# Kernel tuning notes

Hardware: AMD Instinct MI355X
Metric: run time of the kernel (lower is better)

Reference implementation:

```python
import jax, jax.numpy as jnp
import numpy as np

D_MODEL = 768
N_HEADS = 12
D_HEAD = D_MODEL // N_HEADS

def setup_inputs() -> dict:
    key = jax.random.key(0)
    ks = jax.random.split(key, 5)
    B, T = 2, 4096
    x = jax.random.normal(ks[0], (B, T, D_MODEL), dtype=jnp.float32)
    s_in = 1.0 / np.sqrt(D_MODEL)
    W_qkv = jax.random.normal(ks[1], (D_MODEL, 3 * D_MODEL), dtype=jnp.float32) * s_in
    b_qkv = jnp.zeros((3 * D_MODEL,), dtype=jnp.float32)
    W_proj = jax.random.normal(ks[2], (D_MODEL, D_MODEL), dtype=jnp.float32) * s_in
    b_proj = jnp.zeros((D_MODEL,), dtype=jnp.float32)
    return {"x": x, "W_qkv": W_qkv, "b_qkv": b_qkv, "W_proj": W_proj, "b_proj": b_proj}

def reference(x, W_qkv, b_qkv, W_proj, b_proj):
    B, T, C = x.shape
    qkv = x @ W_qkv + b_qkv                      # [B,T,3C]
    q, k, v = jnp.split(qkv, 3, axis=-1)
    def heads(t):
        return t.reshape(B, T, N_HEADS, D_HEAD).transpose(0, 2, 1, 3)  # [B,H,T,d]
    q, k, v = heads(q), heads(k), heads(v)
    scale = 1.0 / np.sqrt(D_HEAD)
    att = jnp.einsum('bhqd,bhkd->bhqk', q, k) * scale  # [B,H,T,T]
    causal = jnp.tril(jnp.ones((T, T), dtype=bool))
    att = jnp.where(causal[None, None], att, -jnp.inf)
    att = jax.nn.softmax(att, axis=-1)
    y = jnp.einsum('bhqk,bhkd->bhqd', att, v)          # [B,H,T,d]
    y = y.transpose(0, 2, 1, 3).reshape(B, T, C)
    return y @ W_proj + b_proj
```

## Files before the change

kernel.cpp:

```cpp
#include <hip/hip_runtime.h>
#include <hip/hip_bf16.h>

typedef __bf16 bf16_t;
typedef bf16_t bf16x4 __attribute__((ext_vector_type(4)));
typedef bf16_t bf16x8 __attribute__((ext_vector_type(8)));
typedef float  f32x4  __attribute__((ext_vector_type(4)));

#define TSEQ   4096
#define NBATCH 2
#define DMODEL 768
#define NHEADS 12
#define DHEAD  64
#define NTOK   (NBATCH*TSEQ)
#define NQKV   (3*DMODEL)

#define QSCALE 0.18033688011112042f
#define SMAX 24.0f

__device__ __forceinline__ f32x4 mfma16(bf16x8 a, bf16x8 b, f32x4 c) {
  return __builtin_amdgcn_mfma_f32_16x16x32_bf16(a, b, c, 0, 0, 0);
}

__device__ __forceinline__ void glds16(const bf16_t* g, bf16_t* l) {
  __builtin_amdgcn_global_load_lds(
      (const __attribute__((address_space(1))) void*)g,
      (__attribute__((address_space(3))) void*)l, 16, 0, 0);
}

__global__ void k_cvt(const float* __restrict__ in, bf16_t* __restrict__ out, int n) {
  int i = blockIdx.x * blockDim.x + threadIdx.x;
  if (i < n) out[i] = (bf16_t)in[i];
}

__global__ __launch_bounds__(256) void k_transpose_cvt(
    const float* __restrict__ in, bf16_t* __restrict__ out, int R, int C) {
  __shared__ bf16_t tile[64][66];
  const int c0 = blockIdx.x * 64, r0 = blockIdx.y * 64;
  const int tid = threadIdx.x;
  const int r = tid >> 2, cb = (tid & 3) * 16;
  const float* ip = in + (long)(r0 + r) * C + c0 + cb;
#pragma unroll
  for (int k = 0; k < 16; k += 4) {
    float4 v = *(const float4*)(ip + k);
    tile[r][cb + k + 0] = (bf16_t)v.x;
    tile[r][cb + k + 1] = (bf16_t)v.y;
    tile[r][cb + k + 2] = (bf16_t)v.z;
    tile[r][cb + k + 3] = (bf16_t)v.w;
  }
  __syncthreads();
  const int c = tid >> 2, rb = (tid & 3) * 16;
  bf16_t* op = out + (long)(c0 + c) * R + r0 + rb;
  bf16x8 v0, v1;
#pragma unroll
  for (int i = 0; i < 8; ++i) { v0[i] = tile[rb + i][c]; v1[i] = tile[rb + 8 + i][c]; }
  *(bf16x8*)(op) = v0;
  *(bf16x8*)(op + 8) = v1;
}

__device__ __forceinline__ void gemm_core(
    const bf16_t* __restrict__ A, const bf16_t* __restrict__ Bt,
    int m0, int n0, bf16_t* As, bf16_t* Bs, f32x4 acc[2][8]) {
  const int tid  = threadIdx.x;
  const int wave = tid >> 6;
  const int lane = tid & 63;
  const int quad = lane >> 4;
  const int l16  = lane & 15;
  const int srow = lane >> 2;
  const int scol = (lane & 3) * 8;

  const bf16_t* a0 = A + (long)(m0 + wave * 16 + srow) * DMODEL + scol;
  const bf16_t* b0 = Bt + (long)(n0 + wave * 16 + srow) * DMODEL + scol;

  glds16(a0,               As + wave * 16 * 32);
  glds16(a0 + 64 * DMODEL, As + (64 + wave * 16) * 32);
  glds16(b0,               Bs + wave * 16 * 32);
  glds16(b0 + 64 * DMODEL, Bs + (64 + wave * 16) * 32);
  __syncthreads();

  for (int ks = 0; ks < DMODEL / 32; ++ks) {
    const int p = ks & 1;
    if (ks + 1 < DMODEL / 32) {
      const int k1 = (ks + 1) * 32;
      bf16_t* Asx = (p ? As : As + 128 * 32);
      bf16_t* Bsx = (p ? Bs : Bs + 128 * 32);
      glds16(a0 + k1,               Asx + wave * 16 * 32);
      glds16(a0 + 64 * DMODEL + k1, Asx + (64 + wave * 16) * 32);
      glds16(b0 + k1,               Bsx + wave * 16 * 32);
      glds16(b0 + 64 * DMODEL + k1, Bsx + (64 + wave * 16) * 32);
    }
    const bf16_t* Ap = As + p * (128 * 32);
    const bf16_t* Bp = Bs + p * (128 * 32);

    bf16x8 af0 = *(const bf16x8*)(Ap + (wave * 32 + l16) * 32 + quad * 8);
    bf16x8 af1 = *(const bf16x8*)(Ap + (wave * 32 + 16 + l16) * 32 + quad * 8);
#pragma unroll
    for (int nt = 0; nt < 8; ++nt) {
      bf16x8 bfm = *(const bf16x8*)(Bp + (nt * 16 + l16) * 32 + quad * 8);
      acc[0][nt] = mfma16(af0, bfm, acc[0][nt]);
      acc[1][nt] = mfma16(af1, bfm, acc[1][nt]);
    }
    __syncthreads();
  }
}

__global__ __launch_bounds__(256) void k_gemm_qkv(
    const bf16_t* __restrict__ A, const bf16_t* __restrict__ Bt,
    const float* __restrict__ bias,
    bf16_t* __restrict__ Qo, bf16_t* __restrict__ Ko, bf16_t* __restrict__ Vt) {
  __shared__ __align__(16) bf16_t As[2 * 128 * 32];
  __shared__ __align__(16) bf16_t Bs[2 * 128 * 32];
  const int wave = threadIdx.x >> 6;
  const int lane = threadIdx.x & 63;
  const int quad = lane >> 4;
  const int l16  = lane & 15;
  const int m0 = blockIdx.x * 128;
  const int n0 = blockIdx.y * 128;

  f32x4 acc[2][8] = {};
  gemm_core(A, Bt, m0, n0, As, Bs, acc);

#pragma unroll
  for (int s = 0; s < 2; ++s)
#pragma unroll
    for (int nt = 0; nt < 8; ++nt) {
      const int n = n0 + nt * 16 + l16;
      const float bv = bias[n];
      const int mb = m0 + wave * 32 + s * 16 + quad * 4;
      const int b = mb >> 12;
      const int t = mb & 4095;
      if (n < DMODEL) {
        const int h = n >> 6, d = n & 63;
        bf16_t* qp = Qo + (((long)(b * NHEADS + h) * TSEQ + t) << 6) + d;
#pragma unroll
        for (int j = 0; j < 4; ++j)
          qp[(long)j << 6] = (bf16_t)((acc[s][nt][j] + bv) * QSCALE);
      } else if (n < 2 * DMODEL) {
        const int n2 = n - DMODEL, h = n2 >> 6, d = n2 & 63;
        bf16_t* kp = Ko + (((long)(b * NHEADS + h) * TSEQ + t) << 6) + d;
#pragma unroll
        for (int j = 0; j < 4; ++j)
          kp[(long)j << 6] = (bf16_t)(acc[s][nt][j] + bv);
      } else {
        const int n2 = n - 2 * DMODEL, h = n2 >> 6, d = n2 & 63;
        bf16x4 v;
#pragma unroll
        for (int j = 0; j < 4; ++j) v[j] = (bf16_t)(acc[s][nt][j] + bv);
        *(bf16x4*)(Vt + ((long)(b * NHEADS + h) * DHEAD + d) * TSEQ + t) = v;
      }
    }
}

__global__ __launch_bounds__(256) void k_gemm_proj(
    const bf16_t* __restrict__ A, const bf16_t* __restrict__ Bt,
    const float* __restrict__ bias, float* __restrict__ out) {
  __shared__ __align__(16) bf16_t As[2 * 128 * 32];
  __shared__ __align__(16) bf16_t Bs[2 * 128 * 32];
  const int wave = threadIdx.x >> 6;
  const int lane = threadIdx.x & 63;
  const int quad = lane >> 4;
  const int l16  = lane & 15;
  const int m0 = blockIdx.x * 128;
  const int n0 = blockIdx.y * 128;

  f32x4 acc[2][8] = {};
  gemm_core(A, Bt, m0, n0, As, Bs, acc);

#pragma unroll
  for (int s = 0; s < 2; ++s)
#pragma unroll
    for (int nt = 0; nt < 8; ++nt) {
      const int n = n0 + nt * 16 + l16;
      const float bv = bias[n];
#pragma unroll
      for (int j = 0; j < 4; ++j) {
        const int m = m0 + wave * 32 + s * 16 + quad * 4 + j;
        out[(long)m * DMODEL + n] = acc[s][nt][j] + bv;
      }
    }
}

__global__ __launch_bounds__(256, 2) void k_attn(
    const bf16_t* __restrict__ Q, const bf16_t* __restrict__ K,
    const bf16_t* __restrict__ Vt,
    bf16_t* __restrict__ P0, bf16_t* __restrict__ P1,
    float* __restrict__ L0, float* __restrict__ L1) {
  __shared__ __align__(16) bf16_t kbuf[2][64 * 64];
  __shared__ __align__(16) bf16_t vbuf[2][64 * 64];
  const int wave = threadIdx.x >> 6;
  const int lane = threadIdx.x & 63;
  const int quad = lane >> 4;
  const int l16  = lane & 15;
  const int bh = blockIdx.x;
  const int qt = 15 - (blockIdx.y >> 1);
  const int sp = blockIdx.y & 1;
  const int half = 2 * qt + 2;
  const int c0 = sp ? half : 0;
  const int niter = half;
  bf16_t* Pp = sp ? P1 : P0;
  float*  Lp = sp ? L1 : L0;

  const bf16_t* Qh = Q + ((long)bh * TSEQ << 6);
  const bf16_t* Kh = K + ((long)bh * TSEQ << 6);
  const bf16_t* Vh = Vt + (long)bh * DHEAD * TSEQ;

  const int qbase = qt * 256 + wave * 64;

  bf16x8 qf[4][2];
#pragma unroll
  for (int s = 0; s < 4; ++s) {
    const bf16_t* qrow = Qh + ((long)(qbase + s * 16 + l16) << 6);
    qf[s][0] = *(const bf16x8*)(qrow + quad * 8);
    qf[s][1] = *(const bf16x8*)(qrow + 32 + quad * 8);
  }

  f32x4 acc[4][4] = {};
  float lS[4] = {0.f, 0.f, 0.f, 0.f};
  const f32x4 minit = {-SMAX, -SMAX, -SMAX, -SMAX};

  const int kperm = ((l16 >> 2) << 3) + (l16 & 3);
  const int swl = l16 & 7;
  const int srow = lane >> 3;
  const int cV = (lane & 7) ^ (srow & 7);
  const int cK0 = (lane & 7) ^ (srow & 3);
  const int cK1 = cK0 ^ 4;
  const int r0a = wave * 16, r0b = wave * 16 + 8;

  {
    const int k00 = c0 << 6;
    glds16(Kh + ((long)(k00 + r0a + srow) << 6) + cK0 * 8, &kbuf[0][r0a * 64]);
    glds16(Kh + ((long)(k00 + r0b + srow) << 6) + cK1 * 8, &kbuf[0][r0b * 64]);
    glds16(Vh + (long)(r0a + srow) * TSEQ + k00 + cV * 8,  &vbuf[0][r0a * 64]);
    glds16(Vh + (long)(r0b + srow) * TSEQ + k00 + cV * 8,  &vbuf[0][r0b * 64]);
  }
  __syncthreads();

  for (int ci = 0; ci < niter; ++ci) {
    const int p = ci & 1;
    const int k0 = (c0 + ci) << 6;
    if (ci + 1 < niter) {
      const int k1 = k0 + 64;
      glds16(Kh + ((long)(k1 + r0a + srow) << 6) + cK0 * 8, &kbuf[1 - p][r0a * 64]);
      glds16(Kh + ((long)(k1 + r0b + srow) << 6) + cK1 * 8, &kbuf[1 - p][r0b * 64]);
      glds16(Vh + (long)(r0a + srow) * TSEQ + k1 + cV * 8,  &vbuf[1 - p][r0a * 64]);
      glds16(Vh + (long)(r0b + srow) * TSEQ + k1 + cV * 8,  &vbuf[1 - p][r0b * 64]);
    }
    const bf16_t* kb = kbuf[p];
    const bf16_t* vb = vbuf[p];

#pragma unroll
    for (int g = 0; g < 2; ++g) {
      const int rw0 = (g * 32 + kperm) * 64;
      const int rw1 = (g * 32 + 4 + kperm) * 64;
      bf16x8 kf00 = *(const bf16x8*)(kb + rw0 + ((quad ^ swl) << 3));
      bf16x8 kf01 = *(const bf16x8*)(kb + rw0 + (((quad + 4) ^ swl) << 3));
      bf16x8 kf10 = *(const bf16x8*)(kb + rw1 + ((quad ^ swl) << 3));
      bf16x8 kf11 = *(const bf16x8*)(kb + rw1 + (((quad + 4) ^ swl) << 3));
      const bool domask = (k0 + g * 32 + 31 > qbase);

      bf16x8 pf[4];
#pragma unroll
      for (int s = 0; s < 4; ++s) {
        f32x4 st0 = minit, st1 = minit;
        st0 = mfma16(kf00, qf[s][0], st0);
        st0 = mfma16(kf01, qf[s][1], st0);
        st1 = mfma16(kf10, qf[s][0], st1);
        st1 = mfma16(kf11, qf[s][1], st1);
        if (domask) {
          const int qS = qbase + s * 16 + l16;
          const int kb0 = k0 + g * 32 + quad * 8;
#pragma unroll
          for (int j = 0; j < 4; ++j) {
            if (kb0 + j > qS)     st0[j] = -1e30f;
            if (kb0 + 4 + j > qS) st1[j] = -1e30f;
          }
        }
        float rs = 0.f;
#pragma unroll
        for (int j = 0; j < 4; ++j) {
          float e0 = __builtin_amdgcn_exp2f(st0[j]);
          float e1 = __builtin_amdgcn_exp2f(st1[j]);
          rs += e0 + e1;
          pf[s][j]     = (bf16_t)e0;
          pf[s][4 + j] = (bf16_t)e1;
        }
        lS[s] += rs;
      }
#pragma unroll
      for (int dt = 0; dt < 4; ++dt) {
        const int row = dt * 16 + l16;
        bf16x8 vf = *(const bf16x8*)(vb + row * 64 + ((((g << 2) + quad) ^ swl) << 3));
#pragma unroll
        for (int s = 0; s < 4; ++s)
          acc[s][dt] = mfma16(vf, pf[s], acc[s][dt]);
      }
    }
    __syncthreads();
  }

#pragma unroll
  for (int s = 0; s < 4; ++s) {
    lS[s] += __shfl_xor(lS[s], 16);
    lS[s] += __shfl_xor(lS[s], 32);
  }
#pragma unroll
  for (int s = 0; s < 4; ++s) {
    const int qS = qbase + s * 16 + l16;
    bf16_t* prow = Pp + (((long)bh * TSEQ + qS) << 6);
#pragma unroll
    for (int dt = 0; dt < 4; ++dt)
#pragma unroll
      for (int j = 0; j < 4; ++j)
        prow[dt * 16 + quad * 4 + j] = (bf16_t)acc[s][dt][j];
    if (quad == 0) Lp[(long)bh * TSEQ + qS] = lS[s];
  }
}

__global__ __launch_bounds__(128) void k_combine(
    const bf16_t* __restrict__ P0, const bf16_t* __restrict__ P1,
    const float* __restrict__ L0, const float* __restrict__ L1,
    bf16_t* __restrict__ Y) {
  const int row = blockIdx.x;
  const int tid = threadIdx.x;
  if (tid < 96) {
    const int b = row >> 12, q = row & 4095;
    const int h = tid >> 3, d0 = (tid & 7) * 8;
    const long bhq = (long)(b * NHEADS + h) * TSEQ + q;
    const long pidx = (bhq << 6) + d0;
    bf16x8 o0 = *(const bf16x8*)(P0 + pidx);
    bf16x8 o1 = *(const bf16x8*)(P1 + pidx);
    const float inv = 1.f / (L0[bhq] + L1[bhq]);
    bf16x8 r;
#pragma unroll
    for (int i = 0; i < 8; ++i) r[i] = (bf16_t)(((float)o0[i] + (float)o1[i]) * inv);
    *(bf16x8*)(Y + (long)row * DMODEL + tid * 8) = r;
  }
}

extern "C" void kernel_launch(void* const* d_in, const int* in_sizes, int n_in,
                              void* d_out, int out_size, void* d_ws, size_t ws_size,
                              hipStream_t stream) {
  (void)in_sizes; (void)n_in; (void)out_size; (void)ws_size;
  const float* x     = (const float*)d_in[0];
  const float* Wqkv  = (const float*)d_in[1];
  const float* bqkv  = (const float*)d_in[2];
  const float* Wproj = (const float*)d_in[3];
  const float* bproj = (const float*)d_in[4];
  float* out = (float*)d_out;

  char* ws = (char*)d_ws;
  bf16_t* Xb      = (bf16_t*)ws; ws += (long)NTOK * DMODEL * 2;
  bf16_t* wqkv_t  = (bf16_t*)ws; ws += (long)NQKV * DMODEL * 2;
  bf16_t* wproj_t = (bf16_t*)ws; ws += (long)DMODEL * DMODEL * 2;
  bf16_t* Qb      = (bf16_t*)ws; ws += (long)NTOK * DMODEL * 2;
  bf16_t* Kb      = (bf16_t*)ws; ws += (long)NTOK * DMODEL * 2;
  bf16_t* Vtb     = (bf16_t*)ws; ws += (long)NTOK * DMODEL * 2;
  bf16_t* Sb      = (bf16_t*)ws; ws += (long)NTOK * DMODEL * 2;
  bf16_t* P1b     = (bf16_t*)ws; ws += (long)NTOK * DMODEL * 2;
  float*  L0b     = (float*)ws;  ws += (long)NHEADS * NBATCH * TSEQ * 4;
  float*  L1b     = (float*)ws;  ws += (long)NHEADS * NBATCH * TSEQ * 4;
  bf16_t* P0b     = Xb;

  int n1 = NTOK * DMODEL;
  k_cvt<<<(n1 + 255) / 256, 256, 0, stream>>>(x, Xb, n1);
  k_transpose_cvt<<<dim3(NQKV / 64, DMODEL / 64), 256, 0, stream>>>(Wqkv, wqkv_t, DMODEL, NQKV);
  k_transpose_cvt<<<dim3(DMODEL / 64, DMODEL / 64), 256, 0, stream>>>(Wproj, wproj_t, DMODEL, DMODEL);

  k_gemm_qkv<<<dim3(NTOK / 128, NQKV / 128), 256, 0, stream>>>(Xb, wqkv_t, bqkv, Qb, Kb, Vtb);
  k_attn<<<dim3(NBATCH * NHEADS, 32), 256, 0, stream>>>(Qb, Kb, Vtb, P0b, P1b, L0b, L1b);
  k_combine<<<NTOK, 128, 0, stream>>>(P0b, P1b, L0b, L1b, Sb);
  k_gemm_proj<<<dim3(NTOK / 128, DMODEL / 128), 256, 0, stream>>>(Sb, wproj_t, bproj, out);
}
```

Measured before the change: 248.7 us.

## Fuse fp32-to-bf16 input conversion into QKV GEMM and flatten combine kernel

Removes the standalone x conversion kernel. The QKV GEMM now streams fp32 activations into LDS, using an XOR-swizzled layout to avoid bank conflicts, and converts them to bf16 in registers before the MFMA. This drops a full write and re-read of the bf16 copy of x, but doubles the bytes loaded for the A tile across the 18 N-blocks and adds conversion work inside the K loop. The combine kernel is also recast as a flat 256-thread grid with no idle threads.

```diff
diff --git a/kernel.cpp b/kernel.cpp
--- a/kernel.cpp
+++ b/kernel.cpp
@@ -26,10 +26,10 @@
       (const __attribute__((address_space(1))) void*)g,
       (__attribute__((address_space(3))) void*)l, 16, 0, 0);
 }
-
-__global__ void k_cvt(const float* __restrict__ in, bf16_t* __restrict__ out, int n) {
-  int i = blockIdx.x * blockDim.x + threadIdx.x;
-  if (i < n) out[i] = (bf16_t)in[i];
+__device__ __forceinline__ void glds16f(const float* g, float* l) {
+  __builtin_amdgcn_global_load_lds(
+      (const __attribute__((address_space(1))) void*)g,
+      (__attribute__((address_space(3))) void*)l, 16, 0, 0);
 }
 
 __global__ __launch_bounds__(256) void k_transpose_cvt(
@@ -104,10 +104,10 @@
 }
 
 __global__ __launch_bounds__(256) void k_gemm_qkv(
-    const bf16_t* __restrict__ A, const bf16_t* __restrict__ Bt,
+    const float* __restrict__ X, const bf16_t* __restrict__ Bt,
     const float* __restrict__ bias,
     bf16_t* __restrict__ Qo, bf16_t* __restrict__ Ko, bf16_t* __restrict__ Vt) {
-  __shared__ __align__(16) bf16_t As[2 * 128 * 32];
+  __shared__ __align__(16) float  Asf[2 * 128 * 32];
   __shared__ __align__(16) bf16_t Bs[2 * 128 * 32];
   const int wave = threadIdx.x >> 6;
   const int lane = threadIdx.x & 63;
@@ -116,8 +116,57 @@
   const int m0 = blockIdx.x * 128;
   const int n0 = blockIdx.y * 128;
 
+  const int arow = lane >> 3;
+  const int achk = (lane & 7) ^ arow;
+  const float* x0 = X + (long)(m0 + wave * 8 + arow) * DMODEL + achk * 4;
+  const int srow = lane >> 2;
+  const int scol = (lane & 3) * 8;
+  const bf16_t* b0 = Bt + (long)(n0 + wave * 16 + srow) * DMODEL + scol;
+
   f32x4 acc[2][8] = {};
-  gemm_core(A, Bt, m0, n0, As, Bs, acc);
+
+#pragma unroll
+  for (int i = 0; i < 4; ++i)
+    glds16f(x0 + (long)i * 32 * DMODEL, Asf + (i * 32 + wave * 8) * 32);
+  glds16(b0,               Bs + wave * 16 * 32);
+  glds16(b0 + 64 * DMODEL, Bs + (64 + wave * 16) * 32);
+  __syncthreads();
+
+  const int sk = l16 & 7;
+  for (int ks = 0; ks < DMODEL / 32; ++ks) {
+    const int p = ks & 1;
+    if (ks + 1 < DMODEL / 32) {
+      const int k1 = (ks + 1) * 32;
+      float*  Asx = (p ? Asf : Asf + 128 * 32);
+      bf16_t* Bsx = (p ? Bs : Bs + 128 * 32);
+#pragma unroll
+      for (int i = 0; i < 4; ++i)
+        glds16f(x0 + (long)i * 32 * DMODEL + k1, Asx + (i * 32 + wave * 8) * 32);
+      glds16(b0 + k1,               Bsx + wave * 16 * 32);
+      glds16(b0 + 64 * DMODEL + k1, Bsx + (64 + wave * 16) * 32);
+    }
+    const float*  Ap = Asf + p * (128 * 32);
+    const bf16_t* Bp = Bs + p * (128 * 32);
+
+    const int r0 = wave * 32 + l16, r1 = r0 + 16;
+    f32x4 a0lo = *(const f32x4*)(Ap + r0 * 32 + (((2 * quad)     ^ sk) << 2));
+    f32x4 a0hi = *(const f32x4*)(Ap + r0 * 32 + (((2 * quad + 1) ^ sk) << 2));
+    f32x4 a1lo = *(const f32x4*)(Ap + r1 * 32 + (((2 * quad)     ^ sk) << 2));
+    f32x4 a1hi = *(const f32x4*)(Ap + r1 * 32 + (((2 * quad + 1) ^ sk) << 2));
+    bf16x8 af0, af1;
+#pragma unroll
+    for (int j = 0; j < 4; ++j) {
+      af0[j] = (bf16_t)a0lo[j]; af0[4 + j] = (bf16_t)a0hi[j];
+      af1[j] = (bf16_t)a1lo[j]; af1[4 + j] = (bf16_t)a1hi[j];
+    }
+#pragma unroll
+    for (int nt = 0; nt < 8; ++nt) {
+      bf16x8 bfm = *(const bf16x8*)(Bp + (nt * 16 + l16) * 32 + quad * 8);
+      acc[0][nt] = mfma16(af0, bfm, acc[0][nt]);
+      acc[1][nt] = mfma16(af1, bfm, acc[1][nt]);
+    }
+    __syncthreads();
+  }
 
 #pragma unroll
   for (int s = 0; s < 2; ++s)
@@ -315,25 +364,24 @@
   }
 }
 
-__global__ __launch_bounds__(128) void k_combine(
+__global__ __launch_bounds__(256) void k_combine(
     const bf16_t* __restrict__ P0, const bf16_t* __restrict__ P1,
     const float* __restrict__ L0, const float* __restrict__ L1,
     bf16_t* __restrict__ Y) {
-  const int row = blockIdx.x;
-  const int tid = threadIdx.x;
-  if (tid < 96) {
-    const int b = row >> 12, q = row & 4095;
-    const int h = tid >> 3, d0 = (tid & 7) * 8;
-    const long bhq = (long)(b * NHEADS + h) * TSEQ + q;
-    const long pidx = (bhq << 6) + d0;
-    bf16x8 o0 = *(const bf16x8*)(P0 + pidx);
-    bf16x8 o1 = *(const bf16x8*)(P1 + pidx);
-    const float inv = 1.f / (L0[bhq] + L1[bhq]);
-    bf16x8 r;
-#pragma unroll
-    for (int i = 0; i < 8; ++i) r[i] = (bf16_t)(((float)o0[i] + (float)o1[i]) * inv);
-    *(bf16x8*)(Y + (long)row * DMODEL + tid * 8) = r;
-  }
+  const int f = (blockIdx.x * 256 + threadIdx.x) * 8;
+  const int tok = f / DMODEL;
+  const int c = f - tok * DMODEL;
+  const int b = tok >> 12, q = tok & 4095;
+  const int h = c >> 6, d0 = c & 63;
+  const long bhq = (long)(b * NHEADS + h) * TSEQ + q;
+  const long pidx = (bhq << 6) + d0;
+  bf16x8 o0 = *(const bf16x8*)(P0 + pidx);
+  bf16x8 o1 = *(const bf16x8*)(P1 + pidx);
+  const float inv = 1.f / (L0[bhq] + L1[bhq]);
+  bf16x8 r;
+#pragma unroll
+  for (int i = 0; i < 8; ++i) r[i] = (bf16_t)(((float)o0[i] + (float)o1[i]) * inv);
+  *(bf16x8*)(Y + f) = r;
 }
 
 extern "C" void kernel_launch(void* const* d_in, const int* in_sizes, int n_in,
@@ -348,25 +396,22 @@
   float* out = (float*)d_out;
 
   char* ws = (char*)d_ws;
-  bf16_t* Xb      = (bf16_t*)ws; ws += (long)NTOK * DMODEL * 2;
   bf16_t* wqkv_t  = (bf16_t*)ws; ws += (long)NQKV * DMODEL * 2;
   bf16_t* wproj_t = (bf16_t*)ws; ws += (long)DMODEL * DMODEL * 2;
   bf16_t* Qb      = (bf16_t*)ws; ws += (long)NTOK * DMODEL * 2;
   bf16_t* Kb      = (bf16_t*)ws; ws += (long)NTOK * DMODEL * 2;
   bf16_t* Vtb     = (bf16_t*)ws; ws += (long)NTOK * DMODEL * 2;
   bf16_t* Sb      = (bf16_t*)ws; ws += (long)NTOK * DMODEL * 2;
+  bf16_t* P0b     = (bf16_t*)ws; ws += (long)NTOK * DMODEL * 2;
   bf16_t* P1b     = (bf16_t*)ws; ws += (long)NTOK * DMODEL * 2;
   float*  L0b     = (float*)ws;  ws += (long)NHEADS * NBATCH * TSEQ * 4;
   float*  L1b     = (float*)ws;  ws += (long)NHEADS * NBATCH * TSEQ * 4;
-  bf16_t* P0b     = Xb;
-
-  int n1 = NTOK * DMODEL;
-  k_cvt<<<(n1 + 255) / 256, 256, 0, stream>>>(x, Xb, n1);
+
   k_transpose_cvt<<<dim3(NQKV / 64, DMODEL / 64), 256, 0, stream>>>(Wqkv, wqkv_t, DMODEL, NQKV);
   k_transpose_cvt<<<dim3(DMODEL / 64, DMODEL / 64), 256, 0, stream>>>(Wproj, wproj_t, DMODEL, DMODEL);
 
-  k_gemm_qkv<<<dim3(NTOK / 128, NQKV / 128), 256, 0, stream>>>(Xb, wqkv_t, bqkv, Qb, Kb, Vtb);
+  k_gemm_qkv<<<dim3(NTOK / 128, NQKV / 128), 256, 0, stream>>>(x, wqkv_t, bqkv, Qb, Kb, Vtb);
   k_attn<<<dim3(NBATCH * NHEADS, 32), 256, 0, stream>>>(Qb, Kb, Vtb, P0b, P1b, L0b, L1b);
-  k_combine<<<NTOK, 128, 0, stream>>>(P0b, P1b, L0b, L1b, Sb);
+  k_combine<<<(NTOK * DMODEL) / (256 * 8), 256, 0, stream>>>(P0b, P1b, L0b, L1b, Sb);
   k_gemm_proj<<<dim3(NTOK / 128, DMODEL / 128), 256, 0, stream>>>(Sb, wproj_t, bproj, out);
 }
```

New measurement: 233.2 us. -6.2%, faster.
